# Kernel optimization log

Measured on AMD Instinct MI355X. Metric: run time of the kernel, lower is better.

The kernel has to match this reference:

```python
import jax, jax.numpy as jnp
import numpy as np

N, XD, NF, HH, WW = 32, 3, 160, 32, 32
KD, VD = 16, NF // 2            # K=16, V=80
CK, CQ = XD * 3 + NF, XD * 2 + NF  # 169, 166


def concat_elu(x):
    # axis = ndim-3 == channel axis for NCHW
    return jax.nn.elu(jnp.concatenate([x, -x], axis=1))


def nin(x, W, b):
    # 1x1 conv / channel-wise linear: W [out, in], x [n, in, h, w]
    return jnp.einsum('oc,nchw->nohw', W, x) + b[None, :, None, None]


def grn(x, Wi, bi, Wo, bo, a=None, Ws=None, bs=None):
    h = nin(concat_elu(x), Wi, bi)
    if a is not None:
        h = h + nin(concat_elu(a), Ws, bs)
    h = concat_elu(h)  # Dropout2d is identity at inference
    h = nin(h, Wo, bo)
    ga, gb = jnp.split(h, 2, axis=1)
    return x + ga * jax.nn.sigmoid(gb)


def causal_softmax(s, eps=1e-7):
    hw = s.shape[-1]
    mask = jnp.tril(jnp.ones((hw, hw), dtype=bool), -1)  # strictly lower triangular
    s = jnp.where(mask, s, 0.0)               # torch.tril(x, -1): zeros, NOT -inf (faithful)
    w = jax.nn.softmax(s, axis=-1)            # softmax over full row incl. the zeros
    w = jnp.where(mask, w, 0.0)               # re-mask
    return w / (jnp.sum(w, axis=-1, keepdims=True) + eps)  # renormalize


def reference(x, ul, b, gkWi, gkbi, gkWo, gkbo, gqWi, gqbi, gqWo, gqbo, gvWi, gvbi, gvWo, gvbo, nkW, nkb, nqW, nqb, nvW, nvb, goWi, gobi, goWs, gobs, goWo, gobo):
    n, _, h, w = x.shape
    hw = h * w
    ul_b = jnp.concatenate([ul, b], axis=1)      # [n, 166, h, w]
    x_ul_b = jnp.concatenate([x, ul_b], axis=1)  # [n, 169, h, w]
    keys = nin(grn(x_ul_b, gkWi, gkbi, gkWo, gkbo), nkW, nkb).reshape(n, KD, hw)
    queries = nin(grn(ul_b, gqWi, gqbi, gqWo, gqbo), nqW, nqb).reshape(n, KD, hw)
    values = nin(grn(x_ul_b, gvWi, gvbi, gvWo, gvbo), nvW, nvb).reshape(n, VD, hw)
    presoftmax = jnp.einsum('nji,njk->nki', keys, queries)  # [n, hw_q, hw_k]
    att_w = causal_softmax(presoftmax)
    att_v = jnp.einsum('nij,nkj->nki', att_w, values).reshape(n, VD, h, w)
    return grn(ul, goWi, gobi, goWo, gobo, a=att_v, Ws=goWs, bs=gobs)


def setup_inputs():
    key = jax.random.key(0)
    keys = iter(jax.random.split(key, 32))
    def rn(shape, s=1.0):
        return jax.random.normal(next(keys), shape, dtype=jnp.float32) * s
    z = lambda c: jnp.zeros((c,), jnp.float32)
    return dict(
        x=rn((N, XD, HH, WW)), ul=rn((N, NF, HH, WW)), b=rn((N, 2 * XD, HH, WW)),
        gkWi=rn((CK, 2 * CK), 0.05), gkbi=z(CK), gkWo=rn((2 * CK, 2 * CK), 0.05), gkbo=z(2 * CK),
        gqWi=rn((CQ, 2 * CQ), 0.05), gqbi=z(CQ), gqWo=rn((2 * CQ, 2 * CQ), 0.05), gqbo=z(2 * CQ),
        gvWi=rn((CK, 2 * CK), 0.05), gvbi=z(CK), gvWo=rn((2 * CK, 2 * CK), 0.05), gvbo=z(2 * CK),
        nkW=rn((KD, CK), 0.05), nkb=z(KD), nqW=rn((KD, CQ), 0.05), nqb=z(KD),
        nvW=rn((VD, CK), 0.05), nvb=z(VD),
        goWi=rn((NF, 2 * NF), 0.05), gobi=z(NF), goWs=rn((NF, NF), 0.05), gobs=z(NF),
        goWo=rn((2 * NF, 2 * NF), 0.05), gobo=z(2 * NF),
    )
```

## Files before the change

### kernel.cpp

```cpp
#include <hip/hip_runtime.h>
#include <cstddef>
#include <cstdint>

#define HW 1024
#define NBATCH 32

typedef unsigned short ushort_t;
typedef unsigned int uint_t;
typedef short s16x8 __attribute__((ext_vector_type(8)));
typedef float f32x4 __attribute__((ext_vector_type(4)));
typedef float f32x16 __attribute__((ext_vector_type(16)));
typedef unsigned int u32x4 __attribute__((ext_vector_type(4)));

__device__ __forceinline__ float elu1(float z){ return z > 0.f ? z : __expf(z) - 1.f; }
__device__ __forceinline__ float sigm(float z){ return 1.f/(1.f+__expf(-z)); }
__device__ __forceinline__ ushort_t f2bf(float f){
  uint_t u = __builtin_bit_cast(uint_t, f);
  u += 0x7FFFu + ((u >> 16) & 1u);
  return (ushort_t)(u >> 16);
}
__device__ __forceinline__ float bf2f(ushort_t h){
  uint_t u = ((uint_t)h) << 16;
  return __builtin_bit_cast(float, u);
}
__device__ __forceinline__ uint_t cvtpk(float lo, float hi){
  uint_t r;
  asm("v_cvt_pk_bf16_f32 %0, %1, %2" : "=v"(r) : "v"(lo), "v"(hi));
  return r;
}
__device__ __forceinline__ void gload_lds16(const void* g, void* l){
  __builtin_amdgcn_global_load_lds((const __attribute__((address_space(1))) unsigned int*)g,
                                   (__attribute__((address_space(3))) unsigned int*)l, 16, 0, 0);
}

__device__ __forceinline__ const float* src_ptr(const float* x, const float* ul, const float* b,
                                                int n, int c, int gm){
  if (gm == 0){
    if (c < 3)   return x  + ((size_t)n*3   + c)*HW;
    if (c < 163) return ul + ((size_t)n*160 + (c-3))*HW;
    return b + ((size_t)n*6 + (c-163))*HW;
  } else if (gm == 1){
    if (c < 160) return ul + ((size_t)n*160 + c)*HW;
    return b + ((size_t)n*6 + (c-160))*HW;
  }
  return ul + ((size_t)n*160 + c)*HW;
}

template<int GM>
__global__ void k_act(const float* __restrict__ x, const float* __restrict__ ul,
                      const float* __restrict__ b,
                      ushort_t* __restrict__ out, int Cb, int P1, int CP){
  int pxg = blockIdx.x*256 + threadIdx.x;
  int n = pxg >> 10, hw = pxg & 1023;
  int c8 = blockIdx.y*8;
  ushort_t* orow = out + (size_t)pxg * CP;
  ushort_t pbuf[8], nbuf[8];
  #pragma unroll
  for (int j = 0; j < 8; ++j){
    int c = c8 + j;
    float s = 0.f;
    if (c < Cb) s = src_ptr(x, ul, b, n, c, GM)[hw];
    pbuf[j] = f2bf(elu1(s));
    nbuf[j] = f2bf(elu1(-s));
  }
  uint4 up, un;
  up.x = (uint_t)pbuf[0] | ((uint_t)pbuf[1]<<16);
  up.y = (uint_t)pbuf[2] | ((uint_t)pbuf[3]<<16);
  up.z = (uint_t)pbuf[4] | ((uint_t)pbuf[5]<<16);
  up.w = (uint_t)pbuf[6] | ((uint_t)pbuf[7]<<16);
  un.x = (uint_t)nbuf[0] | ((uint_t)nbuf[1]<<16);
  un.y = (uint_t)nbuf[2] | ((uint_t)nbuf[3]<<16);
  un.z = (uint_t)nbuf[4] | ((uint_t)nbuf[5]<<16);
  un.w = (uint_t)nbuf[6] | ((uint_t)nbuf[7]<<16);
  *(uint4*)(orow + c8)      = up;
  *(uint4*)(orow + P1 + c8) = un;
}

struct SPtrs { const float* p[12]; };
struct WCfg  { int dst[12], O[12], Kt[12], K1[12], P1[12], Opad[12], Kpad[12], Oh[12]; };

__global__ void k_wconv(SPtrs sp, WCfg c, ushort_t* __restrict__ Wb){
  int d = blockIdx.y;
  int O = c.O[d], Kt = c.Kt[d], K1 = c.K1[d], P1 = c.P1[d], Op = c.Opad[d], Kp = c.Kpad[d], Oh = c.Oh[d];
  ushort_t* dst = Wb + c.dst[d];
  int total = Op*Kp;
  if (d == 9){
    const float* wi = sp.p[9];
    const float* ws = sp.p[11];
    for (int i = blockIdx.x*256 + threadIdx.x; i < total; i += 32*256){
      int o = i / Kp, kk = i - o*Kp;
      float v = 0.f;
      if (o < O) v = (kk < 320) ? wi[(size_t)o*320 + kk] : ws[(size_t)o*160 + (kk - 320)];
      dst[i] = f2bf(v);
    }
    return;
  }
  const float* src = sp.p[d];
  int K2 = Kt - K1;
  for (int i = blockIdx.x*256 + threadIdx.x; i < total; i += 32*256){
    int o = i / Kp, kk = i - o*Kp;
    int k = (kk < K1) ? kk : ((kk >= P1 && kk < P1 + K2) ? (K1 + kk - P1) : -1);
    int so; bool rv;
    if (Oh > 0){
      if (o < 192){ so = o; rv = (o < Oh); }
      else        { so = Oh + (o - 192); rv = ((o - 192) < Oh); }
    } else { so = o; rv = (o < O); }
    float v = (rv && k >= 0) ? src[(size_t)so*Kt + k] : 0.f;
    dst[i] = f2bf(v);
  }
}

template<int EPI>
__global__ __launch_bounds__(256) void k_gmm2(const ushort_t* __restrict__ Wb,
    const float* __restrict__ bias, const float* __restrict__ bias2,
    const ushort_t* __restrict__ act, void* __restrict__ outv, void* __restrict__ outv2,
    const float* __restrict__ xp, const float* __restrict__ ulp, const float* __restrict__ bp,
    int O, int Kpad, int CP, int OP, int P1o)
{
  __shared__ ushort_t Blds[4][2][2048];
  const int tid = threadIdx.x;
  const int w = tid >> 6, l = tid & 63;
  const int n = blockIdx.x >> 2, hw0 = (blockIdx.x & 3)*256;
  const bool FUSED = (EPI == 5 || EPI == 6);
  const int o0 = blockIdx.y*(FUSED ? 32 : 64);

  const ushort_t* actw = act + (size_t)(n*HW + hw0 + w*64)*CP;
  const ushort_t* Wbo  = Wb + (size_t)o0*Kpad;
  const size_t r2off = FUSED ? (size_t)192*Kpad : (size_t)32*Kpad;

#define STAGE2(bufi, ktv) do { \
    int cl_ = (l & 3) ^ ((l >> 4) & 2); \
    _Pragma("unroll") \
    for (int s_ = 0; s_ < 4; ++s_){ \
      const ushort_t* g_ = actw + (size_t)(s_*16 + (l>>2))*CP + (ktv)*32 + cl_*8; \
      gload_lds16(g_, &Blds[w][bufi][s_*512]); \
    } \
  } while(0)

  f32x4 acc[4][4];
  #pragma unroll
  for (int i = 0; i < 4; ++i)
    #pragma unroll
    for (int j = 0; j < 4; ++j) acc[i][j] = (f32x4){0.f,0.f,0.f,0.f};

  const int NT = Kpad >> 5;
  STAGE2(0, 0);
  for (int kt = 0; kt < NT; ++kt){
    int cur = kt & 1;
    const ushort_t* Ab = Wbo + (size_t)(l&15)*Kpad + kt*32 + (l>>4)*8;
    s16x8 a0 = *(const s16x8*)(Ab);
    s16x8 a1 = *(const s16x8*)(Ab + 16*Kpad);
    s16x8 a2 = *(const s16x8*)(Ab + r2off);
    s16x8 a3 = *(const s16x8*)(Ab + r2off + 16*Kpad);
    if (kt + 1 < NT) STAGE2(cur^1, kt+1);
    asm volatile("s_waitcnt vmcnt(4)" ::: "memory");
    const ushort_t* Bb = &Blds[w][cur][0];
    const int chp = ((l>>4) ^ ((l>>2)&2))*8;
    #pragma unroll
    for (int po = 0; po < 4; ++po){
      s16x8 bv = *(const s16x8*)(Bb + po*512 + (l&15)*32 + chp);
      acc[po][0] = __builtin_amdgcn_mfma_f32_16x16x32_bf16(a0, bv, acc[po][0], 0, 0, 0);
      acc[po][1] = __builtin_amdgcn_mfma_f32_16x16x32_bf16(a1, bv, acc[po][1], 0, 0, 0);
      acc[po][2] = __builtin_amdgcn_mfma_f32_16x16x32_bf16(a2, bv, acc[po][2], 0, 0, 0);
      acc[po][3] = __builtin_amdgcn_mfma_f32_16x16x32_bf16(a3, bv, acc[po][3], 0, 0, 0);
    }
  }
#undef STAGE2

  const int g = l >> 4, cc = l & 15;

  if (FUSED){
    const int gm = P1o;
    #pragma unroll
    for (int oo = 0; oo < 2; ++oo){
      int ch = o0 + oo*16 + g*4;
      #pragma unroll
      for (int po = 0; po < 4; ++po){
        int px = hw0 + w*64 + po*16 + cc;
        size_t pb = (size_t)n*HW + px;
        float rr[4];
        #pragma unroll
        for (int i = 0; i < 4; ++i){
          int c = ch + i;
          float r = 0.f;
          if (c < O){
            float ga = acc[po][oo][i]   + bias[c];
            float gb = acc[po][oo+2][i] + bias[O + c];
            float s  = src_ptr(xp, ulp, bp, n, c, gm)[px];
            r = s + ga*sigm(gb);
          }
          rr[i] = r;
        }
        if (EPI == 5){
          uint2 pk;
          pk.x = (uint_t)f2bf(rr[0]) | ((uint_t)f2bf(rr[1])<<16);
          pk.y = (uint_t)f2bf(rr[2]) | ((uint_t)f2bf(rr[3])<<16);
          *(uint2*)((ushort_t*)outv + pb*OP + ch) = pk;
        } else {
          #pragma unroll
          for (int i = 0; i < 4; ++i)
            if (ch + i < O) ((float*)outv)[((size_t)n*O + ch + i)*HW + px] = rr[i];
        }
      }
    }
    return;
  }

  #pragma unroll
  for (int oo = 0; oo < 4; ++oo){
    int ch = o0 + oo*16 + g*4;
    int c = ch;
    const float* bsp = bias;
    ushort_t* oP = (ushort_t*)outv;
    if (EPI == 8 && ch >= 192){ c = ch - 192; bsp = bias2; oP = (ushort_t*)outv2; }
    if (c >= O) continue;
    float b0 = bsp[c];
    float b1 = (c+1 < O) ? bsp[c+1] : 0.f;
    float b2 = (c+2 < O) ? bsp[c+2] : 0.f;
    float b3 = (c+3 < O) ? bsp[c+3] : 0.f;
    if (EPI == 7){
      b0 += bias2[c];
      if (c+1 < O) b1 += bias2[c+1];
      if (c+2 < O) b2 += bias2[c+2];
      if (c+3 < O) b3 += bias2[c+3];
    }
    #pragma unroll
    for (int po = 0; po < 4; ++po){
      int px = hw0 + w*64 + po*16 + cc;
      size_t pb = (size_t)n*HW + px;
      f32x4 a = acc[po][oo];
      float h0 = a[0]+b0, h1 = a[1]+b1, h2v = a[2]+b2, h3 = a[3]+b3;
      if (EPI == 1){
        uint2 pk;
        pk.x = (uint_t)f2bf(h0)  | ((uint_t)f2bf(h1)<<16);
        pk.y = (uint_t)f2bf(h2v) | ((uint_t)f2bf(h3)<<16);
        *(uint2*)(oP + pb*OP + c) = pk;
      } else if (EPI == 2 || EPI == 7 || EPI == 8){
        ushort_t* op = oP + pb*OP;
        uint2 pp, pn;
        pp.x = (uint_t)f2bf(elu1(h0))  | ((uint_t)f2bf(elu1(h1))<<16);
        pp.y = (uint_t)f2bf(elu1(h2v)) | ((uint_t)f2bf(elu1(h3))<<16);
        pn.x = (uint_t)f2bf(elu1(-h0))  | ((uint_t)f2bf(elu1(-h1))<<16);
        pn.y = (uint_t)f2bf(elu1(-h2v)) | ((uint_t)f2bf(elu1(-h3))<<16);
        *(uint2*)(op + c) = pp;
        *(uint2*)(op + P1o + c) = pn;
      } else {
        float hv[4] = {h0, h1, h2v, h3};
        #pragma unroll
        for (int i = 0; i < 4; ++i)
          if (c + i < O) oP[((size_t)n*OP + c + i)*HW + px] = f2bf(hv[i]);
      }
    }
  }
}

__global__ __launch_bounds__(64) void k_attn2(const ushort_t* __restrict__ Kp,
    const ushort_t* __restrict__ Qp, const ushort_t* __restrict__ Vc, ushort_t* __restrict__ Mb){
  const int l = threadIdx.x;
  const int qt = blockIdx.x, n = blockIdx.y;
  const int hi = l >> 5, qcol = l & 31;
  const int qg = qt*32 + qcol;

  s16x8 bq = *(const s16x8*)(Qp + ((size_t)(n*HW + qg))*16 + hi*8);

  f32x16 acc0, acc1, acc2;
  #pragma unroll
  for (int r = 0; r < 16; ++r){ acc0[r]=0.f; acc1[r]=0.f; acc2[r]=0.f; }
  float m = 0.f, S = 0.f;
  const int nkt = qt + 1;

  for (int kt = 0; kt < nkt; ++kt){
    const int j0 = kt*32;
    s16x8 ak = *(const s16x8*)(Kp + ((size_t)(n*HW + j0 + qcol))*16 + hi*8);
    f32x16 zc;
    #pragma unroll
    for (int r = 0; r < 16; ++r) zc[r] = 0.f;
    f32x16 p = __builtin_amdgcn_mfma_f32_32x32x16_bf16(ak, bq, zc, 0, 0, 0);

    float ps[16];
    float tmax = -3.0e38f;
    const bool diag = (kt == qt);
    #pragma unroll
    for (int r = 0; r < 16; ++r){
      int kk = j0 + (r&3) + 8*(r>>2) + 4*hi;
      float sv = p[r];
      if (diag && kk >= qg) sv = -3.0e38f;
      ps[r] = sv;
      tmax = fmaxf(tmax, sv);
    }
    tmax = fmaxf(tmax, __shfl_xor(tmax, 32));
    if (tmax > m + 8.f){
      float f = __expf(m - tmax);
      S *= f;
      #pragma unroll
      for (int r = 0; r < 16; ++r){ acc0[r]*=f; acc1[r]*=f; acc2[r]*=f; }
      m = tmax;
    }
    float pe[16], ts = 0.f;
    #pragma unroll
    for (int r = 0; r < 16; ++r){ pe[r] = __expf(ps[r] - m); ts += pe[r]; }
    S += ts + __shfl_xor(ts, 32);

    uint_t w0 = cvtpk(pe[0],  pe[1]),  w1 = cvtpk(pe[2],  pe[3]);
    uint_t w2 = cvtpk(pe[4],  pe[5]),  w3 = cvtpk(pe[6],  pe[7]);
    uint_t w4 = cvtpk(pe[8],  pe[9]),  w5 = cvtpk(pe[10], pe[11]);
    uint_t w6 = cvtpk(pe[12], pe[13]), w7 = cvtpk(pe[14], pe[15]);
    uint_t o0 = __shfl_xor((int)w0, 32), o1 = __shfl_xor((int)w1, 32);
    uint_t o2 = __shfl_xor((int)w2, 32), o3 = __shfl_xor((int)w3, 32);
    uint_t o4 = __shfl_xor((int)w4, 32), o5 = __shfl_xor((int)w5, 32);
    uint_t o6 = __shfl_xor((int)w6, 32), o7 = __shfl_xor((int)w7, 32);
    u32x4 f0, f1;
    f0.x = hi ? o2 : w0; f0.y = hi ? o3 : w1; f0.z = hi ? w2 : o0; f0.w = hi ? w3 : o1;
    f1.x = hi ? o6 : w4; f1.y = hi ? o7 : w5; f1.z = hi ? w6 : o4; f1.w = hi ? w7 : o5;
    s16x8 pb0 = __builtin_bit_cast(s16x8, f0);
    s16x8 pb1 = __builtin_bit_cast(s16x8, f1);

    const ushort_t* vb = Vc + ((size_t)(n*96 + qcol))*HW + j0 + hi*8;
    s16x8 v00 = *(const s16x8*)(vb);
    s16x8 v01 = *(const s16x8*)(vb + 16);
    s16x8 v10 = *(const s16x8*)(vb + 32*HW);
    s16x8 v11 = *(const s16x8*)(vb + 32*HW + 16);
    s16x8 v20 = *(const s16x8*)(vb + 64*HW);
    s16x8 v21 = *(const s16x8*)(vb + 64*HW + 16);
    acc0 = __builtin_amdgcn_mfma_f32_32x32x16_bf16(v00, pb0, acc0, 0, 0, 0);
    acc0 = __builtin_amdgcn_mfma_f32_32x32x16_bf16(v01, pb1, acc0, 0, 0, 0);
    acc1 = __builtin_amdgcn_mfma_f32_32x32x16_bf16(v10, pb0, acc1, 0, 0, 0);
    acc1 = __builtin_amdgcn_mfma_f32_32x32x16_bf16(v11, pb1, acc1, 0, 0, 0);
    acc2 = __builtin_amdgcn_mfma_f32_32x32x16_bf16(v20, pb0, acc2, 0, 0, 0);
    acc2 = __builtin_amdgcn_mfma_f32_32x32x16_bf16(v21, pb1, acc2, 0, 0, 0);
  }

  float Z = S + (float)(HW - qg)*__expf(-m);
  float inv = 1.f/(S + 1e-7f*Z);
  ushort_t* mrow = Mb + (size_t)(n*HW + qg)*480 + 320;
  #pragma unroll
  for (int rg = 0; rg < 4; ++rg){
    int vb = 8*rg + 4*hi;
    float a0v[4], a1v[4];
    #pragma unroll
    for (int i = 0; i < 4; ++i){ a0v[i] = acc0[4*rg+i]*inv; a1v[i] = acc1[4*rg+i]*inv; }
    uint2 pp, pn;
    pp.x = (uint_t)f2bf(elu1(a0v[0]))  | ((uint_t)f2bf(elu1(a0v[1]))<<16);
    pp.y = (uint_t)f2bf(elu1(a0v[2]))  | ((uint_t)f2bf(elu1(a0v[3]))<<16);
    pn.x = (uint_t)f2bf(elu1(-a0v[0])) | ((uint_t)f2bf(elu1(-a0v[1]))<<16);
    pn.y = (uint_t)f2bf(elu1(-a0v[2])) | ((uint_t)f2bf(elu1(-a0v[3]))<<16);
    *(uint2*)(mrow + vb) = pp;
    *(uint2*)(mrow + 80 + vb) = pn;
    pp.x = (uint_t)f2bf(elu1(a1v[0]))  | ((uint_t)f2bf(elu1(a1v[1]))<<16);
    pp.y = (uint_t)f2bf(elu1(a1v[2]))  | ((uint_t)f2bf(elu1(a1v[3]))<<16);
    pn.x = (uint_t)f2bf(elu1(-a1v[0])) | ((uint_t)f2bf(elu1(-a1v[1]))<<16);
    pn.y = (uint_t)f2bf(elu1(-a1v[2])) | ((uint_t)f2bf(elu1(-a1v[3]))<<16);
    *(uint2*)(mrow + 32 + vb) = pp;
    *(uint2*)(mrow + 112 + vb) = pn;
    if (rg < 2){
      float a2v[4];
      #pragma unroll
      for (int i = 0; i < 4; ++i) a2v[i] = acc2[4*rg+i]*inv;
      pp.x = (uint_t)f2bf(elu1(a2v[0]))  | ((uint_t)f2bf(elu1(a2v[1]))<<16);
      pp.y = (uint_t)f2bf(elu1(a2v[2]))  | ((uint_t)f2bf(elu1(a2v[3]))<<16);
      pn.x = (uint_t)f2bf(elu1(-a2v[0])) | ((uint_t)f2bf(elu1(-a2v[1]))<<16);
      pn.y = (uint_t)f2bf(elu1(-a2v[2])) | ((uint_t)f2bf(elu1(-a2v[3]))<<16);
      *(uint2*)(mrow + 64 + vb) = pp;
      *(uint2*)(mrow + 144 + vb) = pn;
    }
  }
}

extern "C" void kernel_launch(void* const* d_in, const int* in_sizes, int n_in,
                              void* d_out, int out_size, void* d_ws, size_t ws_size,
                              hipStream_t stream) {
  const float* x    = (const float*)d_in[0];
  const float* ul   = (const float*)d_in[1];
  const float* bb   = (const float*)d_in[2];
  const float* gkWi = (const float*)d_in[3];  const float* gkbi = (const float*)d_in[4];
  const float* gkWo = (const float*)d_in[5];  const float* gkbo = (const float*)d_in[6];
  const float* gqWi = (const float*)d_in[7];  const float* gqbi = (const float*)d_in[8];
  const float* gqWo = (const float*)d_in[9];  const float* gqbo = (const float*)d_in[10];
  const float* gvWi = (const float*)d_in[11]; const float* gvbi = (const float*)d_in[12];
  const float* gvWo = (const float*)d_in[13]; const float* gvbo = (const float*)d_in[14];
  const float* nkW  = (const float*)d_in[15]; const float* nkb  = (const float*)d_in[16];
  const float* nqW  = (const float*)d_in[17]; const float* nqb  = (const float*)d_in[18];
  const float* nvW  = (const float*)d_in[19]; const float* nvb  = (const float*)d_in[20];
  const float* goWi = (const float*)d_in[21]; const float* gobi = (const float*)d_in[22];
  const float* goWs = (const float*)d_in[23]; const float* gobs = (const float*)d_in[24];
  const float* goWo = (const float*)d_in[25]; const float* gobo = (const float*)d_in[26];
  float* outp = (float*)d_out;
  char* wsb = (char*)d_ws;

  ushort_t* R0  = (ushort_t*)(wsb + 0);
  ushort_t* R1k = (ushort_t*)(wsb + 23068672);
  ushort_t* R1v = (ushort_t*)(wsb + 46137344);
  ushort_t* R3  = (ushort_t*)(wsb + 69206016);
  ushort_t* Kp  = (ushort_t*)(wsb + 81788928);
  ushort_t* Qp  = (ushort_t*)(wsb + 82837504);
  ushort_t* Vc  = (ushort_t*)(wsb + 83886080);
  ushort_t* M   = (ushort_t*)(wsb + 90177536);
  ushort_t* R2  = (ushort_t*)(wsb + 121634816);
  ushort_t* Wb  = (ushort_t*)(wsb + 142606336);

  static const int dDst[12] = {0,67584,135168,270336,405504,417792,442368,509952,645120,657408,749568,0};
  static const int dO[12]   = {169,169,338,338,16,80,166,332,16,160,320,0};
  static const int dKt[12]  = {338,338,338,338,169,169,332,332,166,0,320,0};
  static const int dK1[12]  = {169,169,169,169,169,169,166,166,166,0,320,0};
  static const int dP1[12]  = {176,176,176,176,9999,9999,176,176,9999,0,9999,0};
  static const int dOp[12]  = {192,192,384,384,64,128,192,384,64,192,384,0};
  static const int dKp[12]  = {352,352,352,352,192,192,352,352,192,480,320,0};
  static const int dOh[12]  = {0,0,169,169,0,0,0,166,0,0,160,0};

  SPtrs sp; WCfg wc;
  const float* srcs[12] = {gkWi,gvWi,gkWo,gvWo,nkW,nvW,gqWi,gqWo,nqW,goWi,goWo,goWs};
  for (int i = 0; i < 12; ++i){
    sp.p[i] = srcs[i];
    wc.dst[i]=dDst[i]; wc.O[i]=dO[i]; wc.Kt[i]=dKt[i]; wc.K1[i]=dK1[i];
    wc.P1[i]=dP1[i]; wc.Opad[i]=dOp[i]; wc.Kpad[i]=dKp[i]; wc.Oh[i]=dOh[i];
  }

  dim3 b256(256), b64t(64);
  k_wconv<<<dim3(32,11), b256, 0, stream>>>(sp, wc, Wb);

#define GMM2(EPI, DI, GY, B1, B2, ACT, OUT, OUT2, O_, CP_, OP_, P1O_) \
  k_gmm2<EPI><<<dim3(128, GY), b256, 0, stream>>>( \
    Wb + dDst[DI], B1, B2, (const ushort_t*)(ACT), OUT, OUT2, x, ul, bb, \
    O_, dKp[DI], CP_, OP_, P1O_)

  k_act<0><<<dim3(128,22), b256, 0, stream>>>(x, ul, bb, R0, 169, 176, 352);
  GMM2(8, 0, 6, gkbi, gvbi, R0, R1k, R1v, 169, 352, 352, 176);
  GMM2(5, 2, 6, gkbo, nullptr, R1k, R3, nullptr, 169, 352, 192, 0);
  GMM2(1, 4, 1, nkb, nullptr, R3, Kp, nullptr, 16, 192, 16, 0);
  GMM2(5, 3, 6, gvbo, nullptr, R1v, R3, nullptr, 169, 352, 192, 0);
  GMM2(4, 5, 2, nvb, nullptr, R3, Vc, nullptr, 80, 192, 96, 0);

  k_act<1><<<dim3(128,22), b256, 0, stream>>>(x, ul, bb, R0, 166, 176, 352);
  GMM2(2, 6, 3, gqbi, nullptr, R0, R1k, nullptr, 166, 352, 352, 176);
  GMM2(5, 7, 6, gqbo, nullptr, R1k, R3, nullptr, 166, 352, 192, 1);
  GMM2(1, 8, 1, nqb, nullptr, R3, Qp, nullptr, 16, 192, 16, 0);

  k_act<2><<<dim3(128,20), b256, 0, stream>>>(x, ul, bb, M, 160, 160, 480);

  k_attn2<<<dim3(32, 32), b64t, 0, stream>>>(Kp, Qp, Vc, M);

  GMM2(7, 9, 3, gobi, gobs, M, R2, nullptr, 160, 480, 320, 160);
  GMM2(6, 10, 5, gobo, nullptr, R2, outp, nullptr, 160, 320, 0, 2);
}
```

Before: 445.2 us.

## Split attention key tiles across four waves and stage GEMM epilogues through LDS

The attention kernel now launches four waves per query tile. Each wave handles every fourth key tile, and the partial accumulators and softmax stats are merged through shared memory with online-softmax rescaling. This targets poor occupancy and serial latency from the single-wave causal loop. The GEMM epilogues for the bf16 fused and concat-ELU outputs are staged through the now-free LDS tile (swizzled) so global writes become 16-byte coalesced row stores, and the last k-iteration waits vmcnt(0) before reading LDS. The added LDS round trips and __syncthreads add overhead, and the extra waves raise register and shared-memory pressure.

```diff
diff --git a/kernel.cpp b/kernel.cpp
--- a/kernel.cpp
+++ b/kernel.cpp
@@ -152,8 +152,12 @@
     s16x8 a1 = *(const s16x8*)(Ab + 16*Kpad);
     s16x8 a2 = *(const s16x8*)(Ab + r2off);
     s16x8 a3 = *(const s16x8*)(Ab + r2off + 16*Kpad);
-    if (kt + 1 < NT) STAGE2(cur^1, kt+1);
-    asm volatile("s_waitcnt vmcnt(4)" ::: "memory");
+    if (kt + 1 < NT){
+      STAGE2(cur^1, kt+1);
+      asm volatile("s_waitcnt vmcnt(4)" ::: "memory");
+    } else {
+      asm volatile("s_waitcnt vmcnt(0)" ::: "memory");
+    }
     const ushort_t* Bb = &Blds[w][cur][0];
     const int chp = ((l>>4) ^ ((l>>2)&2))*8;
     #pragma unroll
@@ -168,39 +172,102 @@
 #undef STAGE2
 
   const int g = l >> 4, cc = l & 15;
+  ushort_t* ep = &Blds[w][0][0];
+  const size_t pbase = (size_t)n*HW + hw0 + w*64;
 
   if (FUSED){
     const int gm = P1o;
+    if (EPI == 6){
+      #pragma unroll
+      for (int oo = 0; oo < 2; ++oo){
+        int ch = o0 + oo*16 + g*4;
+        #pragma unroll
+        for (int po = 0; po < 4; ++po){
+          int px = hw0 + w*64 + po*16 + cc;
+          #pragma unroll
+          for (int i = 0; i < 4; ++i){
+            int c = ch + i;
+            if (c < O){
+              float ga = acc[po][oo][i]   + bias[c];
+              float gb = acc[po][oo+2][i] + bias[O + c];
+              float s  = src_ptr(xp, ulp, bp, n, c, gm)[px];
+              ((float*)outv)[((size_t)n*O + c)*HW + px] = s + ga*sigm(gb);
+            }
+          }
+        }
+      }
+      return;
+    }
     #pragma unroll
     for (int oo = 0; oo < 2; ++oo){
-      int ch = o0 + oo*16 + g*4;
       #pragma unroll
       for (int po = 0; po < 4; ++po){
-        int px = hw0 + w*64 + po*16 + cc;
-        size_t pb = (size_t)n*HW + px;
+        int px = po*16 + cc;
+        int pxg = hw0 + w*64 + px;
         float rr[4];
         #pragma unroll
         for (int i = 0; i < 4; ++i){
-          int c = ch + i;
+          int c = o0 + oo*16 + g*4 + i;
           float r = 0.f;
           if (c < O){
             float ga = acc[po][oo][i]   + bias[c];
             float gb = acc[po][oo+2][i] + bias[O + c];
-            float s  = src_ptr(xp, ulp, bp, n, c, gm)[px];
+            float s  = src_ptr(xp, ulp, bp, n, c, gm)[pxg];
             r = s + ga*sigm(gb);
           }
           rr[i] = r;
         }
-        if (EPI == 5){
+        uint2 pk;
+        pk.x = (uint_t)f2bf(rr[0]) | ((uint_t)f2bf(rr[1])<<16);
+        pk.y = (uint_t)f2bf(rr[2]) | ((uint_t)f2bf(rr[3])<<16);
+        *(uint2*)(ep + px*40 + oo*16 + g*4) = pk;
+      }
+    }
+    #pragma unroll
+    for (int it = 0; it < 4; ++it){
+      int row = it*16 + (l>>2), ch = (l&3)*8;
+      s16x8 v = *(const s16x8*)(ep + row*40 + ch);
+      *(s16x8*)((ushort_t*)outv + (pbase + row)*OP + o0 + ch) = v;
+    }
+    return;
+  }
+
+  if (EPI == 2 || EPI == 7 || EPI == 8){
+    ushort_t* oP = (ushort_t*)outv;
+    const float* bsp = bias;
+    int c0 = o0;
+    if (EPI == 8 && o0 >= 192){ oP = (ushort_t*)outv2; bsp = bias2; c0 = o0 - 192; }
+    #pragma unroll
+    for (int round = 0; round < 2; ++round){
+      int cb = round ? (P1o + c0) : c0;
+      int maxc = (round ? OP : P1o) - cb; if (maxc > 64) maxc = 64;
+      #pragma unroll
+      for (int oo = 0; oo < 4; ++oo){
+        #pragma unroll
+        for (int po = 0; po < 4; ++po){
+          int px = po*16 + cc;
+          float ev[4];
+          #pragma unroll
+          for (int i = 0; i < 4; ++i){
+            int c = c0 + oo*16 + g*4 + i;
+            float bv = 0.f;
+            if (c < O){ bv = bsp[c]; if (EPI == 7) bv += bias2[c]; }
+            float h = acc[po][oo][i] + bv;
+            ev[i] = elu1(round ? -h : h);
+          }
           uint2 pk;
-          pk.x = (uint_t)f2bf(rr[0]) | ((uint_t)f2bf(rr[1])<<16);
-          pk.y = (uint_t)f2bf(rr[2]) | ((uint_t)f2bf(rr[3])<<16);
-          *(uint2*)((ushort_t*)outv + pb*OP + ch) = pk;
-        } else {
-          #pragma unroll
-          for (int i = 0; i < 4; ++i)
-            if (ch + i < O) ((float*)outv)[((size_t)n*O + ch + i)*HW + px] = rr[i];
+          pk.x = (uint_t)f2bf(ev[0]) | ((uint_t)f2bf(ev[1])<<16);
+          pk.y = (uint_t)f2bf(ev[2]) | ((uint_t)f2bf(ev[3])<<16);
+          int off = oo*16 + g*4;
+          *(uint2*)(ep + px*64 + (off ^ ((px&7)<<3))) = pk;
         }
+      }
+      #pragma unroll
+      for (int it = 0; it < 8; ++it){
+        int row = it*8 + (l>>3), ch = (l&7)*8;
+        s16x8 v = *(const s16x8*)(ep + row*64 + (ch ^ ((row&7)<<3)));
+        if (ch < maxc)
+          *(s16x8*)(oP + (pbase + row)*OP + cb + ch) = v;
       }
     }
     return;
@@ -209,21 +276,11 @@
   #pragma unroll
   for (int oo = 0; oo < 4; ++oo){
     int ch = o0 + oo*16 + g*4;
-    int c = ch;
-    const float* bsp = bias;
-    ushort_t* oP = (ushort_t*)outv;
-    if (EPI == 8 && ch >= 192){ c = ch - 192; bsp = bias2; oP = (ushort_t*)outv2; }
-    if (c >= O) continue;
-    float b0 = bsp[c];
-    float b1 = (c+1 < O) ? bsp[c+1] : 0.f;
-    float b2 = (c+2 < O) ? bsp[c+2] : 0.f;
-    float b3 = (c+3 < O) ? bsp[c+3] : 0.f;
-    if (EPI == 7){
-      b0 += bias2[c];
-      if (c+1 < O) b1 += bias2[c+1];
-      if (c+2 < O) b2 += bias2[c+2];
-      if (c+3 < O) b3 += bias2[c+3];
-    }
+    if (ch >= O) continue;
+    float b0 = bias[ch];
+    float b1 = (ch+1 < O) ? bias[ch+1] : 0.f;
+    float b2 = (ch+2 < O) ? bias[ch+2] : 0.f;
+    float b3 = (ch+3 < O) ? bias[ch+3] : 0.f;
     #pragma unroll
     for (int po = 0; po < 4; ++po){
       int px = hw0 + w*64 + po*16 + cc;
@@ -234,29 +291,22 @@
         uint2 pk;
         pk.x = (uint_t)f2bf(h0)  | ((uint_t)f2bf(h1)<<16);
         pk.y = (uint_t)f2bf(h2v) | ((uint_t)f2bf(h3)<<16);
-        *(uint2*)(oP + pb*OP + c) = pk;
-      } else if (EPI == 2 || EPI == 7 || EPI == 8){
-        ushort_t* op = oP + pb*OP;
-        uint2 pp, pn;
-        pp.x = (uint_t)f2bf(elu1(h0))  | ((uint_t)f2bf(elu1(h1))<<16);
-        pp.y = (uint_t)f2bf(elu1(h2v)) | ((uint_t)f2bf(elu1(h3))<<16);
-        pn.x = (uint_t)f2bf(elu1(-h0))  | ((uint_t)f2bf(elu1(-h1))<<16);
-        pn.y = (uint_t)f2bf(elu1(-h2v)) | ((uint_t)f2bf(elu1(-h3))<<16);
-        *(uint2*)(op + c) = pp;
-        *(uint2*)(op + P1o + c) = pn;
+        *(uint2*)((ushort_t*)outv + pb*OP + ch) = pk;
       } else {
         float hv[4] = {h0, h1, h2v, h3};
         #pragma unroll
         for (int i = 0; i < 4; ++i)
-          if (c + i < O) oP[((size_t)n*OP + c + i)*HW + px] = f2bf(hv[i]);
+          if (ch + i < O) ((ushort_t*)outv)[((size_t)n*OP + ch + i)*HW + px] = f2bf(hv[i]);
       }
     }
   }
 }
 
-__global__ __launch_bounds__(64) void k_attn2(const ushort_t* __restrict__ Kp,
+__global__ __launch_bounds__(256) void k_attn2(const ushort_t* __restrict__ Kp,
     const ushort_t* __restrict__ Qp, const ushort_t* __restrict__ Vc, ushort_t* __restrict__ Mb){
-  const int l = threadIdx.x;
+  __shared__ float cmb[3][64][52];
+  const int tid = threadIdx.x;
+  const int wv = tid >> 6, l = tid & 63;
   const int qt = blockIdx.x, n = blockIdx.y;
   const int hi = l >> 5, qcol = l & 31;
   const int qg = qt*32 + qcol;
@@ -267,9 +317,8 @@
   #pragma unroll
   for (int r = 0; r < 16; ++r){ acc0[r]=0.f; acc1[r]=0.f; acc2[r]=0.f; }
   float m = 0.f, S = 0.f;
-  const int nkt = qt + 1;
-
-  for (int kt = 0; kt < nkt; ++kt){
+
+  for (int kt = wv; kt <= qt; kt += 4){
     const int j0 = kt*32;
     s16x8 ak = *(const s16x8*)(Kp + ((size_t)(n*HW + j0 + qcol))*16 + hi*8);
     f32x16 zc;
@@ -328,6 +377,31 @@
     acc1 = __builtin_amdgcn_mfma_f32_32x32x16_bf16(v11, pb1, acc1, 0, 0, 0);
     acc2 = __builtin_amdgcn_mfma_f32_32x32x16_bf16(v20, pb0, acc2, 0, 0, 0);
     acc2 = __builtin_amdgcn_mfma_f32_32x32x16_bf16(v21, pb1, acc2, 0, 0, 0);
+  }
+
+  if (wv){
+    float* d = &cmb[wv-1][l][0];
+    #pragma unroll
+    for (int r = 0; r < 16; ++r){ d[r] = acc0[r]; d[16+r] = acc1[r]; d[32+r] = acc2[r]; }
+    d[48] = m; d[49] = S;
+  }
+  __syncthreads();
+  if (wv) return;
+
+  #pragma unroll
+  for (int w2 = 0; w2 < 3; ++w2){
+    const float* s2 = &cmb[w2][l][0];
+    float m2 = s2[48], S2 = s2[49];
+    float M = fmaxf(m, m2);
+    float f1 = __expf(m - M), f2 = __expf(m2 - M);
+    S = S*f1 + S2*f2;
+    #pragma unroll
+    for (int r = 0; r < 16; ++r){
+      acc0[r] = acc0[r]*f1 + s2[r]*f2;
+      acc1[r] = acc1[r]*f1 + s2[16+r]*f2;
+      acc2[r] = acc2[r]*f1 + s2[32+r]*f2;
+    }
+    m = M;
   }
 
   float Z = S + (float)(HW - qg)*__expf(-m);
@@ -415,7 +489,7 @@
     wc.P1[i]=dP1[i]; wc.Opad[i]=dOp[i]; wc.Kpad[i]=dKp[i]; wc.Oh[i]=dOh[i];
   }
 
-  dim3 b256(256), b64t(64);
+  dim3 b256(256);
   k_wconv<<<dim3(32,11), b256, 0, stream>>>(sp, wc, Wb);
 
 #define GMM2(EPI, DI, GY, B1, B2, ACT, OUT, OUT2, O_, CP_, OP_, P1O_) \
@@ -437,7 +511,7 @@
 
   k_act<2><<<dim3(128,20), b256, 0, stream>>>(x, ul, bb, M, 160, 160, 480);
 
-  k_attn2<<<dim3(32, 32), b64t, 0, stream>>>(Kp, Qp, Vc, M);
+  k_attn2<<<dim3(32, 32), b256, 0, stream>>>(Kp, Qp, Vc, M);
 
   GMM2(7, 9, 3, gobi, gobs, M, R2, nullptr, 160, 480, 320, 160);
   GMM2(6, 10, 5, gobo, nullptr, R2, outp, nullptr, 160, 320, 0, 2);
```

New measurement: 447.0 us. About the same (+0.4%).
